# Optimization experiments

Measured on AMD Instinct MI355X. Metric: run time of the kernel, lower is better.

## Reference

```python
import jax, jax.numpy as jnp
import numpy as np

D_MODEL = 1024
NUM_HEADS = 16
D_K = D_MODEL // NUM_HEADS  # 64
THETA = 10000.0
B = 2
L = 2048


def _rope(x, positions):
    # x: [B, H, L, d_k], positions: [B, L]
    half = D_K // 2
    freqs = 1.0 / (THETA ** (jnp.arange(0, D_K, 2, dtype=jnp.float32) / D_K))  # [half]
    angles = positions.astype(jnp.float32)[..., None] * freqs  # [B, L, half]
    cos = jnp.cos(angles)[:, None, :, :]  # [B, 1, L, half]
    sin = jnp.sin(angles)[:, None, :, :]
    x_even = x[..., 0::2]
    x_odd = x[..., 1::2]
    r_even = x_even * cos - x_odd * sin
    r_odd = x_even * sin + x_odd * cos
    # interleave back: [..., half, 2] -> [..., d_k]
    return jnp.stack([r_even, r_odd], axis=-1).reshape(x.shape)


def setup_inputs() -> dict:
    key = jax.random.key(0)
    ks = jax.random.split(key, 5)
    std = np.sqrt(2.0 / (D_MODEL + D_MODEL))
    x = jax.random.normal(ks[0], (B, L, D_MODEL), dtype=jnp.float32)
    token_positions = jnp.broadcast_to(jnp.arange(L, dtype=jnp.int64 if jax.config.jax_enable_x64 else jnp.int32), (B, L))
    WQ = jax.random.truncated_normal(ks[1], -3.0, 3.0, (D_MODEL, D_MODEL), dtype=jnp.float32) * std
    WK = jax.random.truncated_normal(ks[2], -3.0, 3.0, (D_MODEL, D_MODEL), dtype=jnp.float32) * std
    WV = jax.random.truncated_normal(ks[3], -3.0, 3.0, (D_MODEL, D_MODEL), dtype=jnp.float32) * std
    WO = jax.random.truncated_normal(ks[4], -3.0, 3.0, (D_MODEL, D_MODEL), dtype=jnp.float32) * std
    return {"x": x, "token_positions": token_positions, "WQ": WQ, "WK": WK, "WV": WV, "WO": WO}


def reference(x, token_positions, WQ, WK, WV, WO):
    # Projections: W is [out, in] -> y = x @ W.T
    Q = jnp.einsum('bld,ed->ble', x, WQ)
    K = jnp.einsum('bld,ed->ble', x, WK)
    V = jnp.einsum('bld,ed->ble', x, WV)
    # [B, L, H*d] -> [B, H, L, d]
    def split_heads(t):
        return t.reshape(B, L, NUM_HEADS, D_K).transpose(0, 2, 1, 3)
    Q, K, V = split_heads(Q), split_heads(K), split_heads(V)
    Q = _rope(Q, token_positions)
    K = _rope(K, token_positions)
    scores = jnp.einsum('bhqd,bhkd->bhqk', Q, K) / np.sqrt(D_K).astype(np.float32)
    causal = jnp.tril(jnp.ones((L, L), dtype=bool))
    scores = jnp.where(causal, scores, -jnp.inf)
    attn = jax.nn.softmax(scores, axis=-1)
    out = jnp.einsum('bhqk,bhkd->bhqd', attn, V)  # [B, H, L, d]
    out = out.transpose(0, 2, 1, 3).reshape(B, L, D_MODEL)
    return jnp.einsum('bld,ed->ble', out, WO)
```

## Files before the change

kernel.cpp:

```cpp
#include <hip/hip_runtime.h>
#include <cstdint>
#include <cstddef>

#define D_MODEL 1024
#define NHEAD   16
#define DKH     64
#define BATCH   2
#define SEQ     2048
#define BL      (BATCH*SEQ)

typedef unsigned short u16;
typedef unsigned int   u32;
typedef __bf16 bf16_t;
typedef bf16_t bf16x8 __attribute__((ext_vector_type(8)));
typedef u16    u16x8  __attribute__((ext_vector_type(8)));
typedef u32    u32x4  __attribute__((ext_vector_type(4)));
typedef float  f32x4  __attribute__((ext_vector_type(4)));
typedef float  f32x16 __attribute__((ext_vector_type(16)));

__device__ __forceinline__ u16 f2bf(float f) {
  u32 u = __builtin_bit_cast(u32, f);
  u32 r = (u + 0x7FFFu + ((u >> 16) & 1u)) >> 16;
  return (u16)r;
}
__device__ __forceinline__ float bf2f(u16 h) {
  u32 u = ((u32)h) << 16;
  return __builtin_bit_cast(float, u);
}
__device__ __forceinline__ bf16x8 ldb8(const u16* p) {
  return __builtin_bit_cast(bf16x8, *(const u16x8*)p);
}
__device__ __forceinline__ void gl_lds16(const u16* g, u16* l) {
  __builtin_amdgcn_global_load_lds((const __attribute__((address_space(1))) void*)g,
                                   (__attribute__((address_space(3))) void*)l, 16, 0, 0);
}
#define MFMA16x16x32(a,b,c) __builtin_amdgcn_mfma_f32_16x16x32_bf16((a),(b),(c),0,0,0)
#define MFMA32x32x16(a,b,c) __builtin_amdgcn_mfma_f32_32x32x16_bf16((a),(b),(c),0,0,0)

__global__ void __launch_bounds__(256) cvt1_kernel(const float* __restrict__ in, u16* __restrict__ out, int n8) {
  int i = blockIdx.x * 256 + threadIdx.x;
  if (i >= n8) return;
  float4 a = ((const float4*)in)[2*i];
  float4 b = ((const float4*)in)[2*i+1];
  u16x8 o;
  o[0]=f2bf(a.x); o[1]=f2bf(a.y); o[2]=f2bf(a.z); o[3]=f2bf(a.w);
  o[4]=f2bf(b.x); o[5]=f2bf(b.y); o[6]=f2bf(b.z); o[7]=f2bf(b.w);
  ((u16x8*)out)[i] = o;
}

__global__ void __launch_bounds__(256) cvt4_kernel(const float* __restrict__ i0, const float* __restrict__ i1,
                                                   const float* __restrict__ i2, const float* __restrict__ i3,
                                                   u16* __restrict__ o0, u16* __restrict__ o1,
                                                   u16* __restrict__ o2, u16* __restrict__ o3, int n8) {
  int i = blockIdx.x * 256 + threadIdx.x;
  if (i >= n8) return;
  const float* in = (blockIdx.y == 0) ? i0 : (blockIdx.y == 1) ? i1 : (blockIdx.y == 2) ? i2 : i3;
  u16*        out = (blockIdx.y == 0) ? o0 : (blockIdx.y == 1) ? o1 : (blockIdx.y == 2) ? o2 : o3;
  float4 a = ((const float4*)in)[2*i];
  float4 b = ((const float4*)in)[2*i+1];
  u16x8 o;
  o[0]=f2bf(a.x); o[1]=f2bf(a.y); o[2]=f2bf(a.z); o[3]=f2bf(a.w);
  o[4]=f2bf(b.x); o[5]=f2bf(b.y); o[6]=f2bf(b.z); o[7]=f2bf(b.w);
  ((u16x8*)out)[i] = o;
}

template<bool F32OUT>
__device__ __forceinline__ void gemm_body(const u16* __restrict__ A, const u16* __restrict__ W,
                                          void* __restrict__ Cv, int M, int N, int K) {
  __shared__ u16 Als[128*64];
  __shared__ u16 Bls[128*64];
  const int tid = threadIdx.x, lane = tid & 63, w = tid >> 6;
  const int wr = w >> 1, wc = w & 1;
  const int lr = lane & 15, lg = lane >> 4;
  const int m0 = blockIdx.x * 128, n0 = blockIdx.y * 128;
  f32x4 acc[4][4] = {};
  const int srow = lane >> 3;
  const int scol = (lane & 7) * 8;
  for (int k0 = 0; k0 < K; k0 += 64) {
    __syncthreads();
    #pragma unroll
    for (int c = 0; c < 4; ++c) {
      const int rb = w*32 + c*8;
      const u16* ga = A + (size_t)(m0 + rb + srow)*K + k0 + scol;
      const u16* gb = W + (size_t)(n0 + rb + srow)*K + k0 + scol;
      gl_lds16(ga, &Als[rb*64]);
      gl_lds16(gb, &Bls[rb*64]);
    }
    __syncthreads();
    #pragma unroll
    for (int ks = 0; ks < 2; ++ks) {
      bf16x8 am[4], bn[4];
      #pragma unroll
      for (int f = 0; f < 4; ++f) {
        am[f] = ldb8(&Als[(wr*64 + f*16 + lr)*64 + ks*32 + lg*8]);
        bn[f] = ldb8(&Bls[(wc*64 + f*16 + lr)*64 + ks*32 + lg*8]);
      }
      #pragma unroll
      for (int fm = 0; fm < 4; ++fm)
        #pragma unroll
        for (int fn = 0; fn < 4; ++fn)
          acc[fm][fn] = MFMA16x16x32(am[fm], bn[fn], acc[fm][fn]);
    }
  }
  #pragma unroll
  for (int fm = 0; fm < 4; ++fm)
    #pragma unroll
    for (int fn = 0; fn < 4; ++fn)
      #pragma unroll
      for (int r = 0; r < 4; ++r) {
        const int row = m0 + wr*64 + fm*16 + lg*4 + r;
        const int col = n0 + wc*64 + fn*16 + lr;
        if constexpr (F32OUT) ((float*)Cv)[(size_t)row*N + col] = acc[fm][fn][r];
        else                  ((u16*)Cv)[(size_t)row*N + col] = f2bf(acc[fm][fn][r]);
      }
}

__global__ void __launch_bounds__(256) gemm_qkv_kernel(const u16* __restrict__ X,
    const u16* __restrict__ Wq, const u16* __restrict__ Wk, const u16* __restrict__ Wv,
    u16* __restrict__ Qo, u16* __restrict__ Ko, u16* __restrict__ Vo) {
  const u16* W = (blockIdx.z == 0) ? Wq : (blockIdx.z == 1) ? Wk : Wv;
  u16*       C = (blockIdx.z == 0) ? Qo : (blockIdx.z == 1) ? Ko : Vo;
  gemm_body<false>(X, W, C, BL, D_MODEL, D_MODEL);
}

__global__ void __launch_bounds__(256) gemm_out_kernel(const u16* __restrict__ A, const u16* __restrict__ W,
                                                       float* __restrict__ C) {
  gemm_body<true>(A, W, C, BL, D_MODEL, D_MODEL);
}

__global__ void __launch_bounds__(256) rope_kernel(u16* __restrict__ Q, u16* __restrict__ K,
                                                   const int* __restrict__ pos) {
  int t = blockIdx.x * 256 + threadIdx.x;
  int i  = t & 31;
  int h  = (t >> 5) & 15;
  int bl = t >> 9;
  float fr = exp2f(-(float)i * 0.41524101186092f);
  float ang = (float)pos[bl] * fr;
  float sv, cv;
  sincosf(ang, &sv, &cv);
  const float QS = 0.18033688011112042f;
  size_t base = (size_t)bl * D_MODEL + h * DKH + 2*i;
  u32 qv = *(u32*)&Q[base];
  float qe = bf2f((u16)(qv & 0xFFFFu)), qo = bf2f((u16)(qv >> 16));
  float re = (qe*cv - qo*sv) * QS;
  float ro = (qe*sv + qo*cv) * QS;
  *(u32*)&Q[base] = (u32)f2bf(re) | ((u32)f2bf(ro) << 16);
  u32 kw = *(u32*)&K[base];
  float ke = bf2f((u16)(kw & 0xFFFFu)), ko = bf2f((u16)(kw >> 16));
  *(u32*)&K[base] = (u32)f2bf(ke*cv - ko*sv) | ((u32)f2bf(ke*sv + ko*cv) << 16);
}

#define VSTR 72

struct AttnLds {
  union {
    struct { u16 K[2][2][64*64]; u16 V[2][2][64*VSTR]; } s;
    float mg[4*64*34];
  } u;
};

__device__ __forceinline__ void attn_pass(
    const int q0, const int T,
    const u16* __restrict__ Qb, const u16* __restrict__ Kb,
    const u16* __restrict__ Vb, u16* __restrict__ Ob,
    AttnLds& sh, const int lane, const int w)
{
  const int wl = w & 3, isB = w >> 2;
  const int l31 = lane & 31, h32 = lane >> 5;
  const int SPLIT = T >> 1;
  const int qw0 = q0 + wl * 32;
  const int srow  = lane >> 3;
  const int scol8 = ((lane & 7) ^ srow) * 8;
  const int t0 = isB ? SPLIT : 0;

  bf16x8 qf[4];
  #pragma unroll
  for (int kc = 0; kc < 4; ++kc)
    qf[kc] = ldb8(Qb + (size_t)(qw0 + l31)*D_MODEL + kc*16 + h32*8);
  f32x16 o0 = {}, o1 = {};
  float mrun = 0.0f, lrun = 0.0f;

  {
    const int kv = t0 * 64;
    #pragma unroll
    for (int c = 0; c < 2; ++c) {
      const int rb = wl*16 + c*8;
      gl_lds16(Kb + (size_t)(kv + rb + srow)*D_MODEL + scol8, &sh.u.s.K[isB][0][rb*64]);
    }
    u16x8 a = *(const u16x8*)(Vb + (size_t)(kv + lane)*D_MODEL + (wl*2)*8);
    u16x8 c = *(const u16x8*)(Vb + (size_t)(kv + lane)*D_MODEL + (wl*2+1)*8);
    #pragma unroll
    for (int j = 0; j < 8; ++j) sh.u.s.V[isB][0][(wl*16 + j)*VSTR + lane] = a[j];
    #pragma unroll
    for (int j = 0; j < 8; ++j) sh.u.s.V[isB][0][(wl*16 + 8 + j)*VSTR + lane] = c[j];
  }
  __syncthreads();

  for (int i = 0; i < SPLIT; ++i) {
    const int buf = i & 1, nbuf = buf ^ 1;
    const bool pf = (i + 1 < SPLIT);
    u16x8 vr0, vr1;
    if (pf) {
      const int kvn = (t0 + i + 1) * 64;
      #pragma unroll
      for (int c = 0; c < 2; ++c) {
        const int rb = wl*16 + c*8;
        gl_lds16(Kb + (size_t)(kvn + rb + srow)*D_MODEL + scol8, &sh.u.s.K[isB][nbuf][rb*64]);
      }
      vr0 = *(const u16x8*)(Vb + (size_t)(kvn + lane)*D_MODEL + (wl*2)*8);
      vr1 = *(const u16x8*)(Vb + (size_t)(kvn + lane)*D_MODEL + (wl*2+1)*8);
    }
    const int kv0 = (t0 + i) * 64;
    if (kv0 <= qw0 + 31) {
      const u16* K0 = sh.u.s.K[isB][buf];
      const u16* V0 = sh.u.s.V[isB][buf];
      f32x16 s[2];
      #pragma unroll
      for (int r = 0; r < 16; ++r) { s[0][r] = -mrun; s[1][r] = -mrun; }
      #pragma unroll
      for (int kc = 0; kc < 4; ++kc) {
        const int sl = ((2*kc + h32) ^ (l31 & 7)) * 8;
        bf16x8 k0 = ldb8(&K0[(l31)*64 + sl]);
        bf16x8 k1 = ldb8(&K0[(32 + l31)*64 + sl]);
        s[0] = MFMA32x32x16(k0, qf[kc], s[0]);
        s[1] = MFMA32x32x16(k1, qf[kc], s[1]);
      }
      if (kv0 + 63 > qw0) {
        const int qrow = qw0 + l31;
        #pragma unroll
        for (int kb = 0; kb < 2; ++kb)
          #pragma unroll
          for (int r = 0; r < 16; ++r) {
            int kp = kv0 + kb*32 + (r&3) + 8*(r>>2) + 4*h32;
            if (kp > qrow) s[kb][r] = -1e30f;
          }
      }
      float t[16];
      #pragma unroll
      for (int j = 0; j < 16; ++j) t[j] = fmaxf(s[0][j], s[1][j]);
      #pragma unroll
      for (int st = 8; st >= 1; st >>= 1)
        #pragma unroll
        for (int j = 0; j < 16; ++j) if (j < st) t[j] = fmaxf(t[j], t[j + st]);
      float mx = t[0];
      mx = fmaxf(mx, __shfl_xor(mx, 32, 64));
      if (!__all(mx <= 8.0f)) {
        const float d  = fmaxf(mx, 0.0f);
        const float al = exp2f(-d);
        #pragma unroll
        for (int r = 0; r < 16; ++r) {
          float ar = __shfl(al, (r&3) + 8*(r>>2) + 4*h32, 64);
          o0[r] *= ar;
          o1[r] *= ar;
        }
        lrun *= al;
        mrun += d;
        #pragma unroll
        for (int kb = 0; kb < 2; ++kb)
          #pragma unroll
          for (int r = 0; r < 16; ++r) s[kb][r] -= d;
      }
      #pragma unroll
      for (int kb = 0; kb < 2; ++kb)
        #pragma unroll
        for (int r = 0; r < 16; ++r)
          s[kb][r] = exp2f(s[kb][r]);
      float us[16];
      #pragma unroll
      for (int j = 0; j < 16; ++j) us[j] = s[0][j] + s[1][j];
      #pragma unroll
      for (int st = 8; st >= 1; st >>= 1)
        #pragma unroll
        for (int j = 0; j < 16; ++j) if (j < st) us[j] += us[j + st];
      float ps = us[0];
      ps += __shfl_xor(ps, 32, 64);
      lrun += ps;
      #pragma unroll
      for (int kb = 0; kb < 2; ++kb) {
        u32 pk[8], sw[8];
        #pragma unroll
        for (int k2 = 0; k2 < 8; ++k2) {
          u32 pk_;
          float lo = s[kb][2*k2], hi = s[kb][2*k2+1];
          asm("v_cvt_pk_bf16_f32 %0, %1, %2" : "=v"(pk_) : "v"(lo), "v"(hi));
          pk[k2] = pk_;
          sw[k2] = (u32)__shfl_xor((int)pk_, 32, 64);
        }
        #pragma unroll
        for (int lm = 0; lm < 2; ++lm) {
          const int c = 2*kb + lm;
          u32x4 fw;
          fw[0] = h32 ? sw[4*lm+2] : pk[4*lm+0];
          fw[1] = h32 ? sw[4*lm+3] : pk[4*lm+1];
          fw[2] = h32 ? pk[4*lm+2] : sw[4*lm+0];
          fw[3] = h32 ? pk[4*lm+3] : sw[4*lm+1];
          bf16x8 pfr = __builtin_bit_cast(bf16x8, fw);
          bf16x8 v0 = ldb8(&V0[(l31)*VSTR + 16*c + 8*h32]);
          bf16x8 v1 = ldb8(&V0[(32 + l31)*VSTR + 16*c + 8*h32]);
          o0 = MFMA32x32x16(pfr, v0, o0);
          o1 = MFMA32x32x16(pfr, v1, o1);
        }
      }
    }
    if (pf) {
      u16* Vtn = sh.u.s.V[isB][nbuf];
      #pragma unroll
      for (int j = 0; j < 8; ++j) Vtn[(wl*16 + j)*VSTR + lane] = vr0[j];
      #pragma unroll
      for (int j = 0; j < 8; ++j) Vtn[(wl*16 + 8 + j)*VSTR + lane] = vr1[j];
    }
    __syncthreads();
  }
  float* mg = sh.u.mg;
  if (isB) {
    float* slot = mg + (size_t)(wl*64 + lane) * 34;
    #pragma unroll
    for (int r = 0; r < 16; ++r) { slot[r] = o0[r]; slot[16 + r] = o1[r]; }
    slot[32] = mrun; slot[33] = lrun;
  }
  __syncthreads();
  if (!isB) {
    const float* slot = mg + (size_t)(wl*64 + lane) * 34;
    const float mB = slot[32], lB = slot[33];
    const float m  = fmaxf(mrun, mB);
    const float eA = exp2f(mrun - m), eB = exp2f(mB - m);
    const float linv = 1.0f / (lrun * eA + lB * eB);
    #pragma unroll
    for (int r = 0; r < 16; ++r) {
      const int rp = (r&3) + 8*(r>>2) + 4*h32;
      const float eAr = __shfl(eA, rp, 64);
      const float eBr = __shfl(eB, rp, 64);
      const float lir = __shfl(linv, rp, 64);
      const float v0 = (o0[r]*eAr + slot[r]*eBr) * lir;
      const float v1 = (o1[r]*eAr + slot[16 + r]*eBr) * lir;
      const size_t grow = (size_t)(qw0 + rp) * D_MODEL;
      Ob[grow + l31]      = f2bf(v0);
      Ob[grow + 32 + l31] = f2bf(v1);
    }
  }
}

__global__ void __launch_bounds__(512) attn_kernel(const u16* __restrict__ Q, const u16* __restrict__ K,
                                                   const u16* __restrict__ V, u16* __restrict__ O) {
  __shared__ AttnLds sh;
  const int tid = threadIdx.x, lane = tid & 63, w = tid >> 6;
  const int n = blockIdx.x;
  const int bh = n & 31;
  const int q = 15 - (n >> 5);
  const int b = bh >> 4, head = bh & 15;
  const size_t headoff = (size_t)b * SEQ * D_MODEL + head * DKH;
  const u16* Qb = Q + headoff;
  const u16* Kb = K + headoff;
  const u16* Vb = V + headoff;
  u16* Ob = (u16*)O + headoff;
  attn_pass(q*128, 2*(q+1), Qb, Kb, Vb, Ob, sh, lane, w);
}

extern "C" void kernel_launch(void* const* d_in, const int* in_sizes, int n_in,
                              void* d_out, int out_size, void* d_ws, size_t ws_size,
                              hipStream_t stream) {
  const float* x  = (const float*)d_in[0];
  const int* pos  = (const int*)d_in[1];
  const float* WQ = (const float*)d_in[2];
  const float* WK = (const float*)d_in[3];
  const float* WV = (const float*)d_in[4];
  const float* WO = (const float*)d_in[5];
  u16* ws = (u16*)d_ws;
  const size_t NX = (size_t)BL * D_MODEL;
  const size_t NW = (size_t)D_MODEL * D_MODEL;
  u16* xb  = ws;
  u16* wqb = xb  + NX;
  u16* wkb = wqb + NW;
  u16* wvb = wkb + NW;
  u16* wob = wvb + NW;
  u16* qb  = wob + NW;
  u16* kb  = qb  + NX;
  u16* vb  = kb  + NX;
  u16* ab  = vb  + NX;

  cvt1_kernel<<<dim3((unsigned)(NX/8/256)), 256, 0, stream>>>(x, xb, (int)(NX/8));
  cvt4_kernel<<<dim3((unsigned)(NW/8/256), 4), 256, 0, stream>>>(WQ, WK, WV, WO, wqb, wkb, wvb, wob, (int)(NW/8));
  gemm_qkv_kernel<<<dim3(BL/128, D_MODEL/128, 3), 256, 0, stream>>>(xb, wqb, wkb, wvb, qb, kb, vb);
  rope_kernel<<<dim3(BL*512/256), 256, 0, stream>>>(qb, kb, pos);
  attn_kernel<<<dim3(512), 512, 0, stream>>>(qb, kb, vb, ab);
  gemm_out_kernel<<<dim3(BL/128, D_MODEL/128), 256, 0, stream>>>(ab, wob, (float*)d_out);
}
```

Measured before the change: 143.6 us.

## Fuse RoPE into QKV GEMM epilogue and XOR-swizzle V tile in LDS

Removes the standalone RoPE kernel and applies the rotary embedding (and the Q scale) inside the QKV projection GEMM epilogue, pairing even and odd columns with a lane shuffle and using fast sincos. This saves a kernel launch and a full read-modify-write pass over Q and K. It also drops the padded V stride in favour of an XOR swizzle, which shrinks the attention LDS footprint while still avoiding bank conflicts. Using __sincosf instead of sincosf may reduce accuracy at large angles, and the epilogue adds per-element transcendental work to the GEMM.

```diff
diff --git a/kernel.cpp b/kernel.cpp
--- a/kernel.cpp
+++ b/kernel.cpp
@@ -66,7 +66,8 @@
 
 template<bool F32OUT>
 __device__ __forceinline__ void gemm_body(const u16* __restrict__ A, const u16* __restrict__ W,
-                                          void* __restrict__ Cv, int M, int N, int K) {
+                                          void* __restrict__ Cv, int M, int N, int K,
+                                          const int* __restrict__ pos, int mode) {
   __shared__ u16 Als[128*64];
   __shared__ u16 Bls[128*64];
   const int tid = threadIdx.x, lane = tid & 63, w = tid >> 6;
@@ -102,6 +103,34 @@
           acc[fm][fn] = MFMA16x16x32(am[fm], bn[fn], acc[fm][fn]);
     }
   }
+  if constexpr (!F32OUT) {
+    if (mode) {
+      const float QS  = 0.18033688011112042f;
+      const float sgn = (lane & 1) ? 1.0f : -1.0f;
+      float fr[4];
+      #pragma unroll
+      for (int fn = 0; fn < 4; ++fn)
+        fr[fn] = exp2f(-(float)((fn*16 + lr) >> 1) * 0.41524101186092f);
+      #pragma unroll
+      for (int fm = 0; fm < 4; ++fm)
+        #pragma unroll
+        for (int r = 0; r < 4; ++r) {
+          const int row = m0 + wr*64 + fm*16 + lg*4 + r;
+          const float p = (float)pos[row];
+          #pragma unroll
+          for (int fn = 0; fn < 4; ++fn) {
+            float sv, cv;
+            __sincosf(p * fr[fn], &sv, &cv);
+            float v  = acc[fm][fn][r];
+            float vp = __shfl_xor(v, 1, 64);
+            float out = v*cv + sgn*vp*sv;
+            if (mode == 1) out *= QS;
+            ((u16*)Cv)[(size_t)row*N + n0 + wc*64 + fn*16 + lr] = f2bf(out);
+          }
+        }
+      return;
+    }
+  }
   #pragma unroll
   for (int fm = 0; fm < 4; ++fm)
     #pragma unroll
@@ -117,44 +146,23 @@
 
 __global__ void __launch_bounds__(256) gemm_qkv_kernel(const u16* __restrict__ X,
     const u16* __restrict__ Wq, const u16* __restrict__ Wk, const u16* __restrict__ Wv,
-    u16* __restrict__ Qo, u16* __restrict__ Ko, u16* __restrict__ Vo) {
+    u16* __restrict__ Qo, u16* __restrict__ Ko, u16* __restrict__ Vo,
+    const int* __restrict__ pos) {
   const u16* W = (blockIdx.z == 0) ? Wq : (blockIdx.z == 1) ? Wk : Wv;
   u16*       C = (blockIdx.z == 0) ? Qo : (blockIdx.z == 1) ? Ko : Vo;
-  gemm_body<false>(X, W, C, BL, D_MODEL, D_MODEL);
+  const int mode = (blockIdx.z == 0) ? 1 : (blockIdx.z == 1) ? 2 : 0;
+  gemm_body<false>(X, W, C, BL, D_MODEL, D_MODEL, pos, mode);
 }
 
 __global__ void __launch_bounds__(256) gemm_out_kernel(const u16* __restrict__ A, const u16* __restrict__ W,
                                                        float* __restrict__ C) {
-  gemm_body<true>(A, W, C, BL, D_MODEL, D_MODEL);
-}
-
-__global__ void __launch_bounds__(256) rope_kernel(u16* __restrict__ Q, u16* __restrict__ K,
-                                                   const int* __restrict__ pos) {
-  int t = blockIdx.x * 256 + threadIdx.x;
-  int i  = t & 31;
-  int h  = (t >> 5) & 15;
-  int bl = t >> 9;
-  float fr = exp2f(-(float)i * 0.41524101186092f);
-  float ang = (float)pos[bl] * fr;
-  float sv, cv;
-  sincosf(ang, &sv, &cv);
-  const float QS = 0.18033688011112042f;
-  size_t base = (size_t)bl * D_MODEL + h * DKH + 2*i;
-  u32 qv = *(u32*)&Q[base];
-  float qe = bf2f((u16)(qv & 0xFFFFu)), qo = bf2f((u16)(qv >> 16));
-  float re = (qe*cv - qo*sv) * QS;
-  float ro = (qe*sv + qo*cv) * QS;
-  *(u32*)&Q[base] = (u32)f2bf(re) | ((u32)f2bf(ro) << 16);
-  u32 kw = *(u32*)&K[base];
-  float ke = bf2f((u16)(kw & 0xFFFFu)), ko = bf2f((u16)(kw >> 16));
-  *(u32*)&K[base] = (u32)f2bf(ke*cv - ko*sv) | ((u32)f2bf(ke*sv + ko*cv) << 16);
-}
-
-#define VSTR 72
+  gemm_body<true>(A, W, C, BL, D_MODEL, D_MODEL, nullptr, 0);
+}
+
 
 struct AttnLds {
   union {
-    struct { u16 K[2][2][64*64]; u16 V[2][2][64*VSTR]; } s;
+    struct { u16 K[2][2][64*64]; u16 V[2][2][64*64]; } s;
     float mg[4*64*34];
   } u;
 };
@@ -172,6 +180,7 @@
   const int srow  = lane >> 3;
   const int scol8 = ((lane & 7) ^ srow) * 8;
   const int t0 = isB ? SPLIT : 0;
+  const int vswz = (l31 & 7) << 3;
 
   bf16x8 qf[4];
   #pragma unroll
@@ -190,9 +199,9 @@
     u16x8 a = *(const u16x8*)(Vb + (size_t)(kv + lane)*D_MODEL + (wl*2)*8);
     u16x8 c = *(const u16x8*)(Vb + (size_t)(kv + lane)*D_MODEL + (wl*2+1)*8);
     #pragma unroll
-    for (int j = 0; j < 8; ++j) sh.u.s.V[isB][0][(wl*16 + j)*VSTR + lane] = a[j];
-    #pragma unroll
-    for (int j = 0; j < 8; ++j) sh.u.s.V[isB][0][(wl*16 + 8 + j)*VSTR + lane] = c[j];
+    for (int j = 0; j < 8; ++j) sh.u.s.V[isB][0][(wl*16 + j)*64 + (lane ^ (j<<3))] = a[j];
+    #pragma unroll
+    for (int j = 0; j < 8; ++j) sh.u.s.V[isB][0][(wl*16 + 8 + j)*64 + (lane ^ (j<<3))] = c[j];
   }
   __syncthreads();
 
@@ -295,8 +304,8 @@
           fw[2] = h32 ? pk[4*lm+2] : sw[4*lm+0];
           fw[3] = h32 ? pk[4*lm+3] : sw[4*lm+1];
           bf16x8 pfr = __builtin_bit_cast(bf16x8, fw);
-          bf16x8 v0 = ldb8(&V0[(l31)*VSTR + 16*c + 8*h32]);
-          bf16x8 v1 = ldb8(&V0[(32 + l31)*VSTR + 16*c + 8*h32]);
+          bf16x8 v0 = ldb8(&V0[(l31)*64 + ((16*c + 8*h32) ^ vswz)]);
+          bf16x8 v1 = ldb8(&V0[(32 + l31)*64 + ((16*c + 8*h32) ^ vswz)]);
           o0 = MFMA32x32x16(pfr, v0, o0);
           o1 = MFMA32x32x16(pfr, v1, o1);
         }
@@ -305,9 +314,9 @@
     if (pf) {
       u16* Vtn = sh.u.s.V[isB][nbuf];
       #pragma unroll
-      for (int j = 0; j < 8; ++j) Vtn[(wl*16 + j)*VSTR + lane] = vr0[j];
-      #pragma unroll
-      for (int j = 0; j < 8; ++j) Vtn[(wl*16 + 8 + j)*VSTR + lane] = vr1[j];
+      for (int j = 0; j < 8; ++j) Vtn[(wl*16 + j)*64 + (lane ^ (j<<3))] = vr0[j];
+      #pragma unroll
+      for (int j = 0; j < 8; ++j) Vtn[(wl*16 + 8 + j)*64 + (lane ^ (j<<3))] = vr1[j];
     }
     __syncthreads();
   }
@@ -380,8 +389,7 @@
 
   cvt1_kernel<<<dim3((unsigned)(NX/8/256)), 256, 0, stream>>>(x, xb, (int)(NX/8));
   cvt4_kernel<<<dim3((unsigned)(NW/8/256), 4), 256, 0, stream>>>(WQ, WK, WV, WO, wqb, wkb, wvb, wob, (int)(NW/8));
-  gemm_qkv_kernel<<<dim3(BL/128, D_MODEL/128, 3), 256, 0, stream>>>(xb, wqb, wkb, wvb, qb, kb, vb);
-  rope_kernel<<<dim3(BL*512/256), 256, 0, stream>>>(qb, kb, pos);
+  gemm_qkv_kernel<<<dim3(BL/128, D_MODEL/128, 3), 256, 0, stream>>>(xb, wqb, wkb, wvb, qb, kb, vb, pos);
   attn_kernel<<<dim3(512), 512, 0, stream>>>(qb, kb, vb, ab);
   gemm_out_kernel<<<dim3(BL/128, D_MODEL/128), 256, 0, stream>>>(ab, wob, (float*)d_out);
 }
```

Measured after the change: 139.5 us. -2.9%, faster.
